# Kernel optimization log

Measured on AMD Instinct MI355X. Metric: run time of the kernel, lower is better.

Reference implementation:

```python
import jax, jax.numpy as jnp
import numpy as np

B, N, K, H = 4, 2048, 48, 128
EDGE = 128
FF = 4 * H
SCALE = 30.0


def setup_inputs() -> dict:
    key = jax.random.key(0)
    ks = jax.random.split(key, 12)
    s = lambda fan_in: 1.0 / np.sqrt(fan_in)
    return {
        "h_V": jax.random.normal(ks[0], (B, N, H), jnp.float32),
        "h_E": jax.random.normal(ks[1], (B, N, K, EDGE), jnp.float32),
        "E_idx": jax.random.randint(ks[2], (B, N, K), 0, N, jnp.int32),
        "mask_V": jnp.ones((B, N), jnp.float32),
        "mask_attend": jnp.ones((B, N, K), jnp.float32),
        "W1_w": jax.random.normal(ks[3], (H + EDGE, H), jnp.float32) * s(H + EDGE),
        "W1_b": jnp.zeros((H,), jnp.float32),
        "W2_w": jax.random.normal(ks[4], (H, H), jnp.float32) * s(H),
        "W2_b": jnp.zeros((H,), jnp.float32),
        "W3_w": jax.random.normal(ks[5], (H, H), jnp.float32) * s(H),
        "W3_b": jnp.zeros((H,), jnp.float32),
        "Win_w": jax.random.normal(ks[6], (H, FF), jnp.float32) * s(H),
        "Win_b": jnp.zeros((FF,), jnp.float32),
        "Wout_w": jax.random.normal(ks[7], (FF, H), jnp.float32) * s(FF),
        "Wout_b": jnp.zeros((H,), jnp.float32),
    }


def reference(h_V, h_E, E_idx, mask_V, mask_attend,
              W1_w, W1_b, W2_w, W2_b, W3_w, W3_b,
              Win_w, Win_b, Wout_w, Wout_b):
    gelu_tanh = lambda x: jax.nn.gelu(x, approximate=True)   # self.act = jax.nn.gelu (default approx)
    gelu_exact = lambda x: jax.nn.gelu(x, approximate=False)  # FFN uses approximate=False

    # gather neighbor node features: [B,N,K,H]
    h_nb = jax.vmap(lambda hv, idx: hv[idx])(h_V, E_idx)
    h_EV = jnp.concatenate([h_nb, h_E], axis=-1)              # [B,N,K,H+EDGE]

    # 3-layer message MLP
    m = gelu_tanh(jnp.einsum('bnkc,ch->bnkh', h_EV, W1_w) + W1_b)
    m = gelu_tanh(jnp.einsum('bnkh,hg->bnkg', m, W2_w) + W2_b)
    m = jnp.einsum('bnkg,gh->bnkh', m, W3_w) + W3_b

    m = mask_attend[..., None] * m
    dh = jnp.sum(m, axis=-2) / SCALE                          # [B,N,H]
    h = h_V + dh                                              # dropout rate 0 (eval)

    # position-wise FFN
    ff = gelu_exact(jnp.einsum('bnh,hf->bnf', h, Win_w) + Win_b)
    dh2 = jnp.einsum('bnf,fh->bnh', ff, Wout_w) + Wout_b
    h = h + dh2

    return mask_V[..., None] * h
```

## Files before the change

### kernel.cpp

```cpp
#include <hip/hip_runtime.h>
#include <hip/hip_bf16.h>
#include <math.h>

typedef __attribute__((ext_vector_type(8))) short bf16x8;
typedef __attribute__((ext_vector_type(4))) float f32x4;

#define MFMA16(a,b,c) __builtin_amdgcn_mfma_f32_16x16x32_bf16((a),(b),(c),0,0,0)

__device__ __forceinline__ unsigned int pack2(float a, float b){
  __hip_bfloat162 h = __float22bfloat162_rn(float2{a, b});
  union { __hip_bfloat162 h; unsigned int u; } v; v.h = h;
  return v.u;
}
__device__ __forceinline__ float bflo(unsigned int u){ union{unsigned int i; float f;} v; v.i = u << 16; return v.f; }
__device__ __forceinline__ float bfhi(unsigned int u){ union{unsigned int i; float f;} v; v.i = u & 0xffff0000u; return v.f; }

__device__ __forceinline__ float gelu_fast_f(float x){
  float e = exp2f(x * -2.4554236f);
  return x * __builtin_amdgcn_rcpf(1.0f + e);
}
__device__ __forceinline__ float gelu_erf_f(float x){
  return 0.5f * x * (1.0f + erff(x * 0.70710678118654752f));
}

__global__ void k_prep(const float* __restrict__ W1, const float* __restrict__ W2,
                       const float* __restrict__ W3, const float* __restrict__ Win,
                       const float* __restrict__ Wout, unsigned short* __restrict__ wt)
{
  int t = blockIdx.x * 256 + threadIdx.x;
  if (t >= 196608) return;
  float v;
  if (t < 32768){            int o = t >> 8,        i = t & 255;         v = W1[i*128 + o]; }
  else if (t < 49152){       int l = t - 32768, o = l >> 7, i = l & 127; v = W2[i*128 + o]; }
  else if (t < 65536){       int l = t - 49152, o = l >> 7, i = l & 127; v = W3[i*128 + o]; }
  else if (t < 131072){      int l = t - 65536, o = l >> 7, i = l & 127; v = Win[i*512 + o]; }
  else {                     int l = t - 131072, o = l >> 9, i = l & 511; v = Wout[i*128 + o]; }
  union { float f; unsigned int u; } w; w.f = v;
  unsigned int r = w.u + 0x7fffu + ((w.u >> 16) & 1u);
  wt[t] = (unsigned short)(r >> 16);
}

__global__ __launch_bounds__(256)
void k_hvp(const float* __restrict__ hV, const unsigned short* __restrict__ wt,
           const float* __restrict__ b1, unsigned short* __restrict__ hVpb)
{
  __shared__ char sH[32*256];
  const int tid = threadIdx.x;
  const int wv  = tid >> 6;
  const int ln  = tid & 63;
  const int l15 = ln & 15;
  const int l4  = ln >> 4;
  const int swz = (l15 & 7) << 4;
  const unsigned short* W1T = wt;
  const int nb = blockIdx.x * 32;

#pragma unroll
  for (int it = 0; it < 2; ++it){
    int cid = tid + it*256;
    int r = cid >> 4, cb = cid & 15;
    const float* src = hV + (size_t)(nb + r)*128 + cb*8;
    float4 a0 = *(const float4*)(src);
    float4 a1 = *(const float4*)(src + 4);
    uint4 w;
    w.x = pack2(a0.x, a0.y); w.y = pack2(a0.z, a0.w);
    w.z = pack2(a1.x, a1.y); w.w = pack2(a1.z, a1.w);
    *(uint4*)(&sH[r*256 + ((cb*16) ^ ((r&7)<<4))]) = w;
  }
  __syncthreads();

  f32x4 acc[2][2];
#pragma unroll
  for (int m = 0; m < 2; ++m){ acc[m][0] = f32x4{0.f,0.f,0.f,0.f}; acc[m][1] = f32x4{0.f,0.f,0.f,0.f}; }
#pragma unroll
  for (int ks = 0; ks < 4; ++ks){
    bf16x8 x0 = *(const bf16x8*)(&sH[(l15)*256      + ((ks*64 + l4*16) ^ swz)]);
    bf16x8 x1 = *(const bf16x8*)(&sH[(16 + l15)*256 + ((ks*64 + l4*16) ^ swz)]);
#pragma unroll
    for (int m = 0; m < 2; ++m){
      int orow = (wv*2 + m)*16 + l15;
      bf16x8 wf = *(const bf16x8*)(W1T + orow*256 + ks*32 + l4*8);
      acc[m][0] = MFMA16(wf, x0, acc[m][0]);
      acc[m][1] = MFMA16(wf, x1, acc[m][1]);
    }
  }
#pragma unroll
  for (int m = 0; m < 2; ++m){
    int och0 = (wv*2 + m)*16 + l4*4;
    float q0 = b1[och0], q1 = b1[och0+1], q2 = b1[och0+2], q3 = b1[och0+3];
#pragma unroll
    for (int nt = 0; nt < 2; ++nt){
      int node = nb + nt*16 + l15;
      uint2 p;
      p.x = pack2(acc[m][nt][0] + q0, acc[m][nt][1] + q1);
      p.y = pack2(acc[m][nt][2] + q2, acc[m][nt][3] + q3);
      *(uint2*)(hVpb + (size_t)node*128 + och0) = p;
    }
  }
}

#define NPB 4
__global__ __launch_bounds__(512, 4)
void k_msg(const float* __restrict__ hE, const int* __restrict__ Eidx,
           const float* __restrict__ maskA, const unsigned short* __restrict__ wt,
           const unsigned short* __restrict__ hVpb, const float* __restrict__ b2,
           float* __restrict__ S, float* __restrict__ msums)
{
  __shared__ char sE[2][12288];
  __shared__ char sM[12288];

  const int tid = threadIdx.x;
  const int wv  = tid >> 6;
  const int ln  = tid & 63;
  const int l15 = ln & 15;
  const int l4  = ln >> 4;
  const int swz = (l15 & 7) << 4;

  const unsigned short* W1T = wt;
  const unsigned short* W2T = wt + 32768;

  bf16x8 w1f[4], w2f[4];
  {
    int orow = wv*16 + l15;
#pragma unroll
    for (int ks = 0; ks < 4; ++ks){
      w1f[ks] = *(const bf16x8*)(W1T + orow*256 + 128 + ks*32 + l4*8);
      w2f[ks] = *(const bf16x8*)(W2T + orow*128 + ks*32 + l4*8);
    }
  }
  const int och0 = wv*16 + l4*4;
  const float4 b2q = *(const float4*)(b2 + och0);

  int xoff[4];
#pragma unroll
  for (int ks = 0; ks < 4; ++ks) xoff[ks] = l15*256 + ((ks*64 + l4*16) ^ swz);
  const int woff  = l15*256 + ((och0*2) ^ swz);
  const int soff0 = (tid>>5)*256 + (((tid&31)*8) ^ (((tid>>5)&7)<<4));

  const int node0 = blockIdx.x * NPB;

  float4 e0, e1, e2;
  int pidx0, pidx1, pidx2; float pmk0, pmk1, pmk2;
  {
    const float4* ef = (const float4*)(hE + (size_t)node0 * 6144);
    e0 = ef[tid]; e1 = ef[tid + 512]; e2 = ef[tid + 1024];
    const int* ip = Eidx + node0*48 + l15;
    pidx0 = ip[0]; pidx1 = ip[16]; pidx2 = ip[32];
    const float* mp = maskA + node0*48 + l15;
    pmk0 = mp[0]; pmk1 = mp[16]; pmk2 = mp[32];
  }

#pragma unroll 1
  for (int i = 0; i < NPB; ++i){
    const int node = node0 + i;
    const size_t bb = ((size_t)(node >> 11)) << 11;
    char* sEc = sE[i & 1];

    const float mk0 = pmk0, mk1 = pmk1, mk2 = pmk2;
    uint2 hp0, hp1, hp2;
    {
      const unsigned short* base = hVpb + bb*128 + och0;
      hp0 = *(const uint2*)(base + (size_t)pidx0 * 128);
      hp1 = *(const uint2*)(base + (size_t)pidx1 * 128);
      hp2 = *(const uint2*)(base + (size_t)pidx2 * 128);
    }
    {
      uint2 p;
      p.x = pack2(e0.x, e0.y); p.y = pack2(e0.z, e0.w);
      *(uint2*)(sEc + soff0) = p;
      p.x = pack2(e1.x, e1.y); p.y = pack2(e1.z, e1.w);
      *(uint2*)(sEc + soff0 + 4096) = p;
      p.x = pack2(e2.x, e2.y); p.y = pack2(e2.z, e2.w);
      *(uint2*)(sEc + soff0 + 8192) = p;
    }
    if (i + 1 < NPB){
      const float4* ef = (const float4*)(hE + (size_t)(node + 1) * 6144);
      e0 = ef[tid]; e1 = ef[tid + 512]; e2 = ef[tid + 1024];
      const int* ip = Eidx + (node+1)*48 + l15;
      pidx0 = ip[0]; pidx1 = ip[16]; pidx2 = ip[32];
      const float* mp = maskA + (node+1)*48 + l15;
      pmk0 = mp[0]; pmk1 = mp[16]; pmk2 = mp[32];
    }
    __syncthreads();

    f32x4 a0 = f32x4{0.f,0.f,0.f,0.f}, a1 = a0, a2 = a0;
#pragma unroll
    for (int ks = 0; ks < 4; ++ks){
      bf16x8 x0 = *(const bf16x8*)(sEc + xoff[ks]);
      bf16x8 x1 = *(const bf16x8*)(sEc + xoff[ks] + 4096);
      bf16x8 x2 = *(const bf16x8*)(sEc + xoff[ks] + 8192);
      a0 = MFMA16(w1f[ks], x0, a0);
      a1 = MFMA16(w1f[ks], x1, a1);
      a2 = MFMA16(w1f[ks], x2, a2);
    }
    {
      uint2 p;
      p.x = pack2(gelu_fast_f(a0[0] + bflo(hp0.x)), gelu_fast_f(a0[1] + bfhi(hp0.x)));
      p.y = pack2(gelu_fast_f(a0[2] + bflo(hp0.y)), gelu_fast_f(a0[3] + bfhi(hp0.y)));
      *(uint2*)(sM + woff) = p;
      p.x = pack2(gelu_fast_f(a1[0] + bflo(hp1.x)), gelu_fast_f(a1[1] + bfhi(hp1.x)));
      p.y = pack2(gelu_fast_f(a1[2] + bflo(hp1.y)), gelu_fast_f(a1[3] + bfhi(hp1.y)));
      *(uint2*)(sM + woff + 4096) = p;
      p.x = pack2(gelu_fast_f(a2[0] + bflo(hp2.x)), gelu_fast_f(a2[1] + bfhi(hp2.x)));
      p.y = pack2(gelu_fast_f(a2[2] + bflo(hp2.y)), gelu_fast_f(a2[3] + bfhi(hp2.y)));
      *(uint2*)(sM + woff + 8192) = p;
    }
    __syncthreads();

    a0 = f32x4{0.f,0.f,0.f,0.f}; a1 = a0; a2 = a0;
#pragma unroll
    for (int ks = 0; ks < 4; ++ks){
      bf16x8 x0 = *(const bf16x8*)(sM + xoff[ks]);
      bf16x8 x1 = *(const bf16x8*)(sM + xoff[ks] + 4096);
      bf16x8 x2 = *(const bf16x8*)(sM + xoff[ks] + 8192);
      a0 = MFMA16(w2f[ks], x0, a0);
      a1 = MFMA16(w2f[ks], x1, a1);
      a2 = MFMA16(w2f[ks], x2, a2);
    }
    {
      float s0, s1, s2, s3;
      s0  = mk0 * gelu_fast_f(a0[0] + b2q.x);
      s1  = mk0 * gelu_fast_f(a0[1] + b2q.y);
      s2  = mk0 * gelu_fast_f(a0[2] + b2q.z);
      s3  = mk0 * gelu_fast_f(a0[3] + b2q.w);
      s0 += mk1 * gelu_fast_f(a1[0] + b2q.x);
      s1 += mk1 * gelu_fast_f(a1[1] + b2q.y);
      s2 += mk1 * gelu_fast_f(a1[2] + b2q.z);
      s3 += mk1 * gelu_fast_f(a1[3] + b2q.w);
      s0 += mk2 * gelu_fast_f(a2[0] + b2q.x);
      s1 += mk2 * gelu_fast_f(a2[1] + b2q.y);
      s2 += mk2 * gelu_fast_f(a2[2] + b2q.z);
      s3 += mk2 * gelu_fast_f(a2[3] + b2q.w);
#pragma unroll
      for (int off = 1; off < 16; off <<= 1){
        s0 += __shfl_xor(s0, off);
        s1 += __shfl_xor(s1, off);
        s2 += __shfl_xor(s2, off);
        s3 += __shfl_xor(s3, off);
      }
      if (l15 == 0){
        float4 o;
        o.x = s0 * (1.0f/30.0f);
        o.y = s1 * (1.0f/30.0f);
        o.z = s2 * (1.0f/30.0f);
        o.w = s3 * (1.0f/30.0f);
        *(float4*)(S + (size_t)node*128 + och0) = o;
      }
      if (wv == 0){
        float q = mk0 + mk1 + mk2;
#pragma unroll
        for (int off = 1; off < 16; off <<= 1) q += __shfl_xor(q, off);
        if (ln == 0) msums[node] = q * (1.0f/30.0f);
      }
    }
  }
}

__global__ __launch_bounds__(256, 2)
void k_ffn(const float* __restrict__ hV, const float* __restrict__ S,
           const float* __restrict__ msums, const float* __restrict__ maskV,
           const unsigned short* __restrict__ wt,
           const float* __restrict__ b3, const float* __restrict__ bin,
           const float* __restrict__ bout, float* __restrict__ out)
{
  __shared__ char  sS[32*256];
  __shared__ char  sH[32*256];
  __shared__ float sHf[32*132];
  __shared__ char  sF[32*1024];

  const int tid = threadIdx.x;
  const int wv  = tid >> 6;
  const int ln  = tid & 63;
  const int l15 = ln & 15;
  const int l4  = ln >> 4;
  const int swz = (l15 & 7) << 4;
  const unsigned short* W3T   = wt + 49152;
  const unsigned short* WinT  = wt + 65536;
  const unsigned short* WoutT = wt + 131072;
  const int nb = blockIdx.x * 32;

#pragma unroll
  for (int it = 0; it < 2; ++it){
    int cid = tid + it*256;
    int r = cid >> 4, cb = cid & 15;
    const float* src = S + (size_t)(nb + r)*128 + cb*8;
    float4 a0 = *(const float4*)(src);
    float4 a1 = *(const float4*)(src + 4);
    uint4 w;
    w.x = pack2(a0.x, a0.y); w.y = pack2(a0.z, a0.w);
    w.z = pack2(a1.x, a1.y); w.w = pack2(a1.z, a1.w);
    *(uint4*)(&sS[r*256 + ((cb*16) ^ ((r&7)<<4))]) = w;
  }
  __syncthreads();

  {
    f32x4 acc[2][2];
#pragma unroll
    for (int m = 0; m < 2; ++m){ acc[m][0] = f32x4{0.f,0.f,0.f,0.f}; acc[m][1] = f32x4{0.f,0.f,0.f,0.f}; }
#pragma unroll
    for (int ks = 0; ks < 4; ++ks){
      bf16x8 x0 = *(const bf16x8*)(&sS[(l15)*256      + ((ks*64 + l4*16) ^ swz)]);
      bf16x8 x1 = *(const bf16x8*)(&sS[(16 + l15)*256 + ((ks*64 + l4*16) ^ swz)]);
#pragma unroll
      for (int m = 0; m < 2; ++m){
        int cr = (wv*2 + m)*16 + l15;
        bf16x8 wf = *(const bf16x8*)(W3T + cr*128 + ks*32 + l4*8);
        acc[m][0] = MFMA16(wf, x0, acc[m][0]);
        acc[m][1] = MFMA16(wf, x1, acc[m][1]);
      }
    }
#pragma unroll
    for (int m = 0; m < 2; ++m){
      int ch0 = (wv*2 + m)*16 + l4*4;
      const float4 b3q = *(const float4*)(b3 + ch0);
#pragma unroll
      for (int nt = 0; nt < 2; ++nt){
        int row  = nt*16 + l15;
        int node = nb + row;
        float ms = msums[node];
        const float4 hv = *(const float4*)(hV + (size_t)node*128 + ch0);
        float h0 = hv.x + acc[m][nt][0] + ms*b3q.x;
        float h1 = hv.y + acc[m][nt][1] + ms*b3q.y;
        float h2 = hv.z + acc[m][nt][2] + ms*b3q.z;
        float h3 = hv.w + acc[m][nt][3] + ms*b3q.w;
        float4 hf; hf.x = h0; hf.y = h1; hf.z = h2; hf.w = h3;
        *(float4*)(&sHf[row*132 + ch0]) = hf;
        uint2 p; p.x = pack2(h0, h1); p.y = pack2(h2, h3);
        *(uint2*)(&sH[row*256 + ((ch0*2) ^ ((row&7)<<4))]) = p;
      }
    }
  }
  __syncthreads();

  f32x4 accA[8][2];
#pragma unroll
  for (int m8 = 0; m8 < 8; ++m8){ accA[m8][0] = f32x4{0.f,0.f,0.f,0.f}; accA[m8][1] = f32x4{0.f,0.f,0.f,0.f}; }
#pragma unroll
  for (int ks = 0; ks < 4; ++ks){
    bf16x8 x0 = *(const bf16x8*)(&sH[(l15)*256      + ((ks*64 + l4*16) ^ swz)]);
    bf16x8 x1 = *(const bf16x8*)(&sH[(16 + l15)*256 + ((ks*64 + l4*16) ^ swz)]);
#pragma unroll
    for (int m8 = 0; m8 < 8; ++m8){
      int fr = (wv*8 + m8)*16 + l15;
      bf16x8 wf = *(const bf16x8*)(WinT + fr*128 + ks*32 + l4*8);
      accA[m8][0] = MFMA16(wf, x0, accA[m8][0]);
      accA[m8][1] = MFMA16(wf, x1, accA[m8][1]);
    }
  }
#pragma unroll
  for (int m8 = 0; m8 < 8; ++m8){
    int f0 = (wv*8 + m8)*16 + l4*4;
    float q0 = bin[f0], q1 = bin[f0+1], q2 = bin[f0+2], q3 = bin[f0+3];
#pragma unroll
    for (int nt = 0; nt < 2; ++nt){
      int row = nt*16 + l15;
      float g0 = gelu_erf_f(accA[m8][nt][0] + q0);
      float g1 = gelu_erf_f(accA[m8][nt][1] + q1);
      float g2 = gelu_erf_f(accA[m8][nt][2] + q2);
      float g3 = gelu_erf_f(accA[m8][nt][3] + q3);
      uint2 p; p.x = pack2(g0, g1); p.y = pack2(g2, g3);
      *(uint2*)(&sF[row*1024 + ((f0*2) ^ swz)]) = p;
    }
  }
  __syncthreads();

  f32x4 accB[2][2];
#pragma unroll
  for (int m = 0; m < 2; ++m){ accB[m][0] = f32x4{0.f,0.f,0.f,0.f}; accB[m][1] = f32x4{0.f,0.f,0.f,0.f}; }
#pragma unroll
  for (int ks = 0; ks < 16; ++ks){
    bf16x8 x0 = *(const bf16x8*)(&sF[(l15)*1024      + ((ks*64 + l4*16) ^ swz)]);
    bf16x8 x1 = *(const bf16x8*)(&sF[(16 + l15)*1024 + ((ks*64 + l4*16) ^ swz)]);
#pragma unroll
    for (int m = 0; m < 2; ++m){
      int cr = (wv*2 + m)*16 + l15;
      bf16x8 wf = *(const bf16x8*)(WoutT + cr*512 + ks*32 + l4*8);
      accB[m][0] = MFMA16(wf, x0, accB[m][0]);
      accB[m][1] = MFMA16(wf, x1, accB[m][1]);
    }
  }
#pragma unroll
  for (int m = 0; m < 2; ++m){
    int ch0 = (wv*2 + m)*16 + l4*4;
    float q0 = bout[ch0], q1 = bout[ch0+1], q2 = bout[ch0+2], q3 = bout[ch0+3];
#pragma unroll
    for (int nt = 0; nt < 2; ++nt){
      int row  = nt*16 + l15;
      int node = nb + row;
      float mv = maskV[node];
      const float4 hf = *(const float4*)(&sHf[row*132 + ch0]);
      float4 o;
      o.x = mv * (hf.x + accB[m][nt][0] + q0);
      o.y = mv * (hf.y + accB[m][nt][1] + q1);
      o.z = mv * (hf.z + accB[m][nt][2] + q2);
      o.w = mv * (hf.w + accB[m][nt][3] + q3);
      *(float4*)(out + (size_t)node*128 + ch0) = o;
    }
  }
}

extern "C" void kernel_launch(void* const* d_in, const int* in_sizes, int n_in,
                              void* d_out, int out_size, void* d_ws, size_t ws_size,
                              hipStream_t stream)
{
  const float* hV    = (const float*)d_in[0];
  const float* hE    = (const float*)d_in[1];
  const int*   Eidx  = (const int*)  d_in[2];
  const float* maskV = (const float*)d_in[3];
  const float* maskA = (const float*)d_in[4];
  const float* W1w = (const float*)d_in[5];
  const float* W1b = (const float*)d_in[6];
  const float* W2w = (const float*)d_in[7];
  const float* W2b = (const float*)d_in[8];
  const float* W3w = (const float*)d_in[9];
  const float* W3b = (const float*)d_in[10];
  const float* Winw  = (const float*)d_in[11];
  const float* Winb  = (const float*)d_in[12];
  const float* Woutw = (const float*)d_in[13];
  const float* Woutb = (const float*)d_in[14];
  float* out = (float*)d_out;

  unsigned short* wt   = (unsigned short*)d_ws;
  unsigned short* hVpb = (unsigned short*)((char*)d_ws + (1u << 19));
  float* Sbuf  = (float*)((char*)d_ws + (1u << 19) + (1u << 21));
  float* msums = (float*)((char*)d_ws + (1u << 19) + (1u << 21) + (1u << 22));

  k_prep<<<dim3(768),  dim3(256), 0, stream>>>(W1w, W2w, W3w, Winw, Woutw, wt);
  k_hvp <<<dim3(256),  dim3(256), 0, stream>>>(hV, wt, W1b, hVpb);
  k_msg <<<dim3(2048), dim3(512), 0, stream>>>(hE, Eidx, maskA, wt, hVpb, W2b, Sbuf, msums);
  k_ffn <<<dim3(256),  dim3(256), 0, stream>>>(hV, Sbuf, msums, maskV, wt, W3b, Winb, Woutb, out);
}
```

Measured before the change: 115.0 us.

## Process one node per block in message kernel, dropping software prefetch loop

The message kernel previously looped over four nodes per block and double-buffered the edge tile, prefetching the next node's edge features into registers. It now handles one node per block, launching four times as many blocks and issuing the edge, index and gather loads up front, before the weight fragment loads. This relies on more resident blocks and hardware scheduling to hide memory latency instead of intra-block prefetch. The cost is that every block reloads the W1/W2 weight fragments, so block launch overhead and weight traffic grow.

```diff
diff --git a/kernel.cpp b/kernel.cpp
--- a/kernel.cpp
+++ b/kernel.cpp
@@ -98,14 +98,13 @@
   }
 }
 
-#define NPB 4
 __global__ __launch_bounds__(512, 4)
 void k_msg(const float* __restrict__ hE, const int* __restrict__ Eidx,
            const float* __restrict__ maskA, const unsigned short* __restrict__ wt,
            const unsigned short* __restrict__ hVpb, const float* __restrict__ b2,
            float* __restrict__ S, float* __restrict__ msums)
 {
-  __shared__ char sE[2][12288];
+  __shared__ char sE[12288];
   __shared__ char sM[12288];
 
   const int tid = threadIdx.x;
@@ -118,6 +117,28 @@
   const unsigned short* W1T = wt;
   const unsigned short* W2T = wt + 32768;
 
+  const int node = blockIdx.x;
+  const size_t bb = ((size_t)(node >> 11)) << 11;
+
+  int   idx0, idx1, idx2;
+  float mk0,  mk1,  mk2;
+  {
+    const int*   ip = Eidx  + node*48 + l15;
+    const float* mp = maskA + node*48 + l15;
+    idx0 = ip[0]; idx1 = ip[16]; idx2 = ip[32];
+    mk0  = mp[0]; mk1  = mp[16]; mk2  = mp[32];
+  }
+  const float4* ef = (const float4*)(hE + (size_t)node * 6144);
+  float4 e0 = ef[tid], e1 = ef[tid + 512], e2 = ef[tid + 1024];
+
+  uint2 hp0, hp1, hp2;
+  {
+    const unsigned short* base = hVpb + bb*128 + wv*16 + l4*4;
+    hp0 = *(const uint2*)(base + (size_t)idx0 * 128);
+    hp1 = *(const uint2*)(base + (size_t)idx1 * 128);
+    hp2 = *(const uint2*)(base + (size_t)idx2 * 128);
+  }
+
   bf16x8 w1f[4], w2f[4];
   {
     int orow = wv*16 + l15;
@@ -136,121 +157,85 @@
   const int woff  = l15*256 + ((och0*2) ^ swz);
   const int soff0 = (tid>>5)*256 + (((tid&31)*8) ^ (((tid>>5)&7)<<4));
 
-  const int node0 = blockIdx.x * NPB;
-
-  float4 e0, e1, e2;
-  int pidx0, pidx1, pidx2; float pmk0, pmk1, pmk2;
-  {
-    const float4* ef = (const float4*)(hE + (size_t)node0 * 6144);
-    e0 = ef[tid]; e1 = ef[tid + 512]; e2 = ef[tid + 1024];
-    const int* ip = Eidx + node0*48 + l15;
-    pidx0 = ip[0]; pidx1 = ip[16]; pidx2 = ip[32];
-    const float* mp = maskA + node0*48 + l15;
-    pmk0 = mp[0]; pmk1 = mp[16]; pmk2 = mp[32];
-  }
-
-#pragma unroll 1
-  for (int i = 0; i < NPB; ++i){
-    const int node = node0 + i;
-    const size_t bb = ((size_t)(node >> 11)) << 11;
-    char* sEc = sE[i & 1];
-
-    const float mk0 = pmk0, mk1 = pmk1, mk2 = pmk2;
-    uint2 hp0, hp1, hp2;
-    {
-      const unsigned short* base = hVpb + bb*128 + och0;
-      hp0 = *(const uint2*)(base + (size_t)pidx0 * 128);
-      hp1 = *(const uint2*)(base + (size_t)pidx1 * 128);
-      hp2 = *(const uint2*)(base + (size_t)pidx2 * 128);
-    }
-    {
-      uint2 p;
-      p.x = pack2(e0.x, e0.y); p.y = pack2(e0.z, e0.w);
-      *(uint2*)(sEc + soff0) = p;
-      p.x = pack2(e1.x, e1.y); p.y = pack2(e1.z, e1.w);
-      *(uint2*)(sEc + soff0 + 4096) = p;
-      p.x = pack2(e2.x, e2.y); p.y = pack2(e2.z, e2.w);
-      *(uint2*)(sEc + soff0 + 8192) = p;
-    }
-    if (i + 1 < NPB){
-      const float4* ef = (const float4*)(hE + (size_t)(node + 1) * 6144);
-      e0 = ef[tid]; e1 = ef[tid + 512]; e2 = ef[tid + 1024];
-      const int* ip = Eidx + (node+1)*48 + l15;
-      pidx0 = ip[0]; pidx1 = ip[16]; pidx2 = ip[32];
-      const float* mp = maskA + (node+1)*48 + l15;
-      pmk0 = mp[0]; pmk1 = mp[16]; pmk2 = mp[32];
-    }
-    __syncthreads();
-
-    f32x4 a0 = f32x4{0.f,0.f,0.f,0.f}, a1 = a0, a2 = a0;
-#pragma unroll
-    for (int ks = 0; ks < 4; ++ks){
-      bf16x8 x0 = *(const bf16x8*)(sEc + xoff[ks]);
-      bf16x8 x1 = *(const bf16x8*)(sEc + xoff[ks] + 4096);
-      bf16x8 x2 = *(const bf16x8*)(sEc + xoff[ks] + 8192);
-      a0 = MFMA16(w1f[ks], x0, a0);
-      a1 = MFMA16(w1f[ks], x1, a1);
-      a2 = MFMA16(w1f[ks], x2, a2);
-    }
-    {
-      uint2 p;
-      p.x = pack2(gelu_fast_f(a0[0] + bflo(hp0.x)), gelu_fast_f(a0[1] + bfhi(hp0.x)));
-      p.y = pack2(gelu_fast_f(a0[2] + bflo(hp0.y)), gelu_fast_f(a0[3] + bfhi(hp0.y)));
-      *(uint2*)(sM + woff) = p;
-      p.x = pack2(gelu_fast_f(a1[0] + bflo(hp1.x)), gelu_fast_f(a1[1] + bfhi(hp1.x)));
-      p.y = pack2(gelu_fast_f(a1[2] + bflo(hp1.y)), gelu_fast_f(a1[3] + bfhi(hp1.y)));
-      *(uint2*)(sM + woff + 4096) = p;
-      p.x = pack2(gelu_fast_f(a2[0] + bflo(hp2.x)), gelu_fast_f(a2[1] + bfhi(hp2.x)));
-      p.y = pack2(gelu_fast_f(a2[2] + bflo(hp2.y)), gelu_fast_f(a2[3] + bfhi(hp2.y)));
-      *(uint2*)(sM + woff + 8192) = p;
-    }
-    __syncthreads();
-
-    a0 = f32x4{0.f,0.f,0.f,0.f}; a1 = a0; a2 = a0;
-#pragma unroll
-    for (int ks = 0; ks < 4; ++ks){
-      bf16x8 x0 = *(const bf16x8*)(sM + xoff[ks]);
-      bf16x8 x1 = *(const bf16x8*)(sM + xoff[ks] + 4096);
-      bf16x8 x2 = *(const bf16x8*)(sM + xoff[ks] + 8192);
-      a0 = MFMA16(w2f[ks], x0, a0);
-      a1 = MFMA16(w2f[ks], x1, a1);
-      a2 = MFMA16(w2f[ks], x2, a2);
-    }
-    {
-      float s0, s1, s2, s3;
-      s0  = mk0 * gelu_fast_f(a0[0] + b2q.x);
-      s1  = mk0 * gelu_fast_f(a0[1] + b2q.y);
-      s2  = mk0 * gelu_fast_f(a0[2] + b2q.z);
-      s3  = mk0 * gelu_fast_f(a0[3] + b2q.w);
-      s0 += mk1 * gelu_fast_f(a1[0] + b2q.x);
-      s1 += mk1 * gelu_fast_f(a1[1] + b2q.y);
-      s2 += mk1 * gelu_fast_f(a1[2] + b2q.z);
-      s3 += mk1 * gelu_fast_f(a1[3] + b2q.w);
-      s0 += mk2 * gelu_fast_f(a2[0] + b2q.x);
-      s1 += mk2 * gelu_fast_f(a2[1] + b2q.y);
-      s2 += mk2 * gelu_fast_f(a2[2] + b2q.z);
-      s3 += mk2 * gelu_fast_f(a2[3] + b2q.w);
-#pragma unroll
-      for (int off = 1; off < 16; off <<= 1){
-        s0 += __shfl_xor(s0, off);
-        s1 += __shfl_xor(s1, off);
-        s2 += __shfl_xor(s2, off);
-        s3 += __shfl_xor(s3, off);
-      }
-      if (l15 == 0){
-        float4 o;
-        o.x = s0 * (1.0f/30.0f);
-        o.y = s1 * (1.0f/30.0f);
-        o.z = s2 * (1.0f/30.0f);
-        o.w = s3 * (1.0f/30.0f);
-        *(float4*)(S + (size_t)node*128 + och0) = o;
-      }
-      if (wv == 0){
-        float q = mk0 + mk1 + mk2;
-#pragma unroll
-        for (int off = 1; off < 16; off <<= 1) q += __shfl_xor(q, off);
-        if (ln == 0) msums[node] = q * (1.0f/30.0f);
-      }
+  {
+    uint2 p;
+    p.x = pack2(e0.x, e0.y); p.y = pack2(e0.z, e0.w);
+    *(uint2*)(sE + soff0) = p;
+    p.x = pack2(e1.x, e1.y); p.y = pack2(e1.z, e1.w);
+    *(uint2*)(sE + soff0 + 4096) = p;
+    p.x = pack2(e2.x, e2.y); p.y = pack2(e2.z, e2.w);
+    *(uint2*)(sE + soff0 + 8192) = p;
+  }
+  __syncthreads();
+
+  f32x4 a0 = f32x4{0.f,0.f,0.f,0.f}, a1 = a0, a2 = a0;
+#pragma unroll
+  for (int ks = 0; ks < 4; ++ks){
+    bf16x8 x0 = *(const bf16x8*)(sE + xoff[ks]);
+    bf16x8 x1 = *(const bf16x8*)(sE + xoff[ks] + 4096);
+    bf16x8 x2 = *(const bf16x8*)(sE + xoff[ks] + 8192);
+    a0 = MFMA16(w1f[ks], x0, a0);
+    a1 = MFMA16(w1f[ks], x1, a1);
+    a2 = MFMA16(w1f[ks], x2, a2);
+  }
+  {
+    uint2 p;
+    p.x = pack2(gelu_fast_f(a0[0] + bflo(hp0.x)), gelu_fast_f(a0[1] + bfhi(hp0.x)));
+    p.y = pack2(gelu_fast_f(a0[2] + bflo(hp0.y)), gelu_fast_f(a0[3] + bfhi(hp0.y)));
+    *(uint2*)(sM + woff) = p;
+    p.x = pack2(gelu_fast_f(a1[0] + bflo(hp1.x)), gelu_fast_f(a1[1] + bfhi(hp1.x)));
+    p.y = pack2(gelu_fast_f(a1[2] + bflo(hp1.y)), gelu_fast_f(a1[3] + bfhi(hp1.y)));
+    *(uint2*)(sM + woff + 4096) = p;
+    p.x = pack2(gelu_fast_f(a2[0] + bflo(hp2.x)), gelu_fast_f(a2[1] + bfhi(hp2.x)));
+    p.y = pack2(gelu_fast_f(a2[2] + bflo(hp2.y)), gelu_fast_f(a2[3] + bfhi(hp2.y)));
+    *(uint2*)(sM + woff + 8192) = p;
+  }
+  __syncthreads();
+
+  a0 = f32x4{0.f,0.f,0.f,0.f}; a1 = a0; a2 = a0;
+#pragma unroll
+  for (int ks = 0; ks < 4; ++ks){
+    bf16x8 x0 = *(const bf16x8*)(sM + xoff[ks]);
+    bf16x8 x1 = *(const bf16x8*)(sM + xoff[ks] + 4096);
+    bf16x8 x2 = *(const bf16x8*)(sM + xoff[ks] + 8192);
+    a0 = MFMA16(w2f[ks], x0, a0);
+    a1 = MFMA16(w2f[ks], x1, a1);
+    a2 = MFMA16(w2f[ks], x2, a2);
+  }
+  {
+    float s0, s1, s2, s3;
+    s0  = mk0 * gelu_fast_f(a0[0] + b2q.x);
+    s1  = mk0 * gelu_fast_f(a0[1] + b2q.y);
+    s2  = mk0 * gelu_fast_f(a0[2] + b2q.z);
+    s3  = mk0 * gelu_fast_f(a0[3] + b2q.w);
+    s0 += mk1 * gelu_fast_f(a1[0] + b2q.x);
+    s1 += mk1 * gelu_fast_f(a1[1] + b2q.y);
+    s2 += mk1 * gelu_fast_f(a1[2] + b2q.z);
+    s3 += mk1 * gelu_fast_f(a1[3] + b2q.w);
+    s0 += mk2 * gelu_fast_f(a2[0] + b2q.x);
+    s1 += mk2 * gelu_fast_f(a2[1] + b2q.y);
+    s2 += mk2 * gelu_fast_f(a2[2] + b2q.z);
+    s3 += mk2 * gelu_fast_f(a2[3] + b2q.w);
+#pragma unroll
+    for (int off = 1; off < 16; off <<= 1){
+      s0 += __shfl_xor(s0, off);
+      s1 += __shfl_xor(s1, off);
+      s2 += __shfl_xor(s2, off);
+      s3 += __shfl_xor(s3, off);
+    }
+    if (l15 == 0){
+      float4 o;
+      o.x = s0 * (1.0f/30.0f);
+      o.y = s1 * (1.0f/30.0f);
+      o.z = s2 * (1.0f/30.0f);
+      o.w = s3 * (1.0f/30.0f);
+      *(float4*)(S + (size_t)node*128 + och0) = o;
+    }
+    if (wv == 0){
+      float q = mk0 + mk1 + mk2;
+#pragma unroll
+      for (int off = 1; off < 16; off <<= 1) q += __shfl_xor(q, off);
+      if (ln == 0) msums[node] = q * (1.0f/30.0f);
     }
   }
 }
@@ -426,6 +411,6 @@
 
   k_prep<<<dim3(768),  dim3(256), 0, stream>>>(W1w, W2w, W3w, Winw, Woutw, wt);
   k_hvp <<<dim3(256),  dim3(256), 0, stream>>>(hV, wt, W1b, hVpb);
-  k_msg <<<dim3(2048), dim3(512), 0, stream>>>(hE, Eidx, maskA, wt, hVpb, W2b, Sbuf, msums);
+  k_msg <<<dim3(8192), dim3(512), 0, stream>>>(hE, Eidx, maskA, wt, hVpb, W2b, Sbuf, msums);
   k_ffn <<<dim3(256),  dim3(256), 0, stream>>>(hV, Sbuf, msums, maskV, wt, W3b, Winb, Woutb, out);
 }
```

After: 125.2 us. +8.9%, slower.
